# Optimization experiments

Measured on AMD Instinct MI355X. Metric: run time of the kernel, lower is better.

Reference implementation:

```python
import jax, jax.numpy as jnp
import numpy as np

NUM_HEADS = 32
NUM_GROUP_HEADS = 8
DIM_MODEL = 2048
DIM_K = 64
DIM_V = 64


def setup_inputs() -> dict:
    key = jax.random.key(0)
    ks = jax.random.split(key, 11)
    B, S = 1, 2048
    scale = 0.02
    inp = {
        "queries": jax.random.normal(ks[0], (B, S, DIM_MODEL), jnp.float32),
        "keys": jax.random.normal(ks[1], (B, S, DIM_MODEL), jnp.float32),
        "values": jax.random.normal(ks[2], (B, S, DIM_MODEL), jnp.float32),
        "Wq": jax.random.normal(ks[3], (DIM_MODEL, DIM_K * NUM_HEADS), jnp.float32) * scale,
        "bq": jnp.zeros((DIM_K * NUM_HEADS,), jnp.float32),
        "Wk": jax.random.normal(ks[4], (DIM_MODEL, DIM_K * NUM_GROUP_HEADS), jnp.float32) * scale,
        "bk": jnp.zeros((DIM_K * NUM_GROUP_HEADS,), jnp.float32),
        "Wv": jax.random.normal(ks[5], (DIM_MODEL, DIM_V * NUM_GROUP_HEADS), jnp.float32) * scale,
        "bv": jnp.zeros((DIM_V * NUM_GROUP_HEADS,), jnp.float32),
        "Wo": jax.random.normal(ks[6], (DIM_V * NUM_HEADS, DIM_MODEL), jnp.float32) * scale,
        "bo": jnp.zeros((DIM_MODEL,), jnp.float32),
    }
    return inp


def reference(queries, keys, values, Wq, bq, Wk, bk, Wv, bv, Wo, bo):
    B, Sq, _ = queries.shape
    _, Sk, _ = keys.shape
    H, G = NUM_HEADS, NUM_GROUP_HEADS
    repeats = H // G

    # projections -> [B, heads, S, d]
    q = (queries @ Wq + bq).reshape(B, Sq, H, DIM_K).transpose(0, 2, 1, 3)
    k = (keys @ Wk + bk).reshape(B, Sk, G, DIM_K).transpose(0, 2, 1, 3)
    v = (values @ Wv + bv).reshape(B, Sk, G, DIM_V).transpose(0, 2, 1, 3)

    # GQA: repeat each group head `repeats` times (repeat_interleave on head dim)
    k = jnp.repeat(k, repeats, axis=1)  # [B, H, Sk, dk]
    v = jnp.repeat(v, repeats, axis=1)  # [B, H, Sk, dv]

    scores = jnp.einsum("bhqd,bhkd->bhqk", q, k) / (DIM_K ** 0.5)
    causal = jnp.triu(jnp.ones((Sq, Sk), dtype=bool), k=1)
    scores = jnp.where(causal, -jnp.inf, scores)
    attn = jax.nn.softmax(scores, axis=-1)
    out = jnp.einsum("bhqk,bhkd->bhqd", attn, v)  # [B, H, Sq, dv]
    out = out.transpose(0, 2, 1, 3).reshape(B, Sq, H * DIM_V)
    return out @ Wo + bo
```

## Files before the change

### kernel.cpp

```cpp
#include <hip/hip_runtime.h>
#include <hip/hip_bf16.h>

#define S_LEN  2048
#define DMODEL 2048
#define NH     32
#define NG     8
#define DK     64
#define DV     64

typedef short bf16x8 __attribute__((ext_vector_type(8)));
typedef float f32x4  __attribute__((ext_vector_type(4)));

__device__ __forceinline__ ushort f32_to_bf16(float f) {
    uint u = __float_as_uint(f);
    return (ushort)((u + 0x7fffu + ((u >> 16) & 1u)) >> 16);
}
__device__ __forceinline__ float bf16_to_f32(ushort h) {
    return __uint_as_float(((uint)h) << 16);
}

__global__ void cast_f32_to_bf16(const float* __restrict__ in,
                                 ushort* __restrict__ out, int n8) {
    int i = blockIdx.x * blockDim.x + threadIdx.x;
    const int stride = gridDim.x * blockDim.x;
    for (; i < n8; i += stride) {
        const float4 a = ((const float4*)in)[2 * i];
        const float4 b = ((const float4*)in)[2 * i + 1];
        uint4 o;
        o.x = (uint)f32_to_bf16(a.x) | ((uint)f32_to_bf16(a.y) << 16);
        o.y = (uint)f32_to_bf16(a.z) | ((uint)f32_to_bf16(a.w) << 16);
        o.z = (uint)f32_to_bf16(b.x) | ((uint)f32_to_bf16(b.y) << 16);
        o.w = (uint)f32_to_bf16(b.z) | ((uint)f32_to_bf16(b.w) << 16);
        ((uint4*)out)[i] = o;
    }
}

__global__ void transpose_cast_bf16(const float* __restrict__ W,
                                    ushort* __restrict__ Wt, int K, int N) {
    __shared__ float t[32][33];
    const int n0 = blockIdx.x * 32, k0 = blockIdx.y * 32;
    const int tx = threadIdx.x, ty = threadIdx.y;
#pragma unroll
    for (int i = 0; i < 4; ++i)
        t[ty + 8 * i][tx] = W[(size_t)(k0 + ty + 8 * i) * N + n0 + tx];
    __syncthreads();
#pragma unroll
    for (int i = 0; i < 4; ++i)
        Wt[(size_t)(n0 + ty + 8 * i) * K + k0 + tx] = f32_to_bf16(t[tx][ty + 8 * i]);
}

__global__ void transpose_bf16(const ushort* __restrict__ in,
                               ushort* __restrict__ out, int R, int C) {
    __shared__ ushort t[32][34];
    const int c0 = blockIdx.x * 32, r0 = blockIdx.y * 32;
    const int tx = threadIdx.x, ty = threadIdx.y;
#pragma unroll
    for (int i = 0; i < 4; ++i)
        t[ty + 8 * i][tx] = in[(size_t)(r0 + ty + 8 * i) * C + c0 + tx];
    __syncthreads();
#pragma unroll
    for (int i = 0; i < 4; ++i)
        out[(size_t)(c0 + ty + 8 * i) * R + r0 + tx] = t[tx][ty + 8 * i];
}

template <bool OUT_F32>
__device__ __forceinline__ void gemm_body_128x64(
        const ushort* __restrict__ A, const ushort* __restrict__ Bt,
        const float* __restrict__ bias, void* __restrict__ Cv,
        ushort* As, ushort* Bs, int N, int K) {
    const int tid  = threadIdx.x;
    const int lane = tid & 63, wave = tid >> 6;
    const int l15 = lane & 15, quad = lane >> 4;
    const int row0 = blockIdx.y * 128, col0 = blockIdx.x * 64;

    f32x4 acc[2][4];
#pragma unroll
    for (int i = 0; i < 2; ++i)
#pragma unroll
        for (int j = 0; j < 4; ++j) { f32x4 z = {0.f,0.f,0.f,0.f}; acc[i][j] = z; }

    const int ar = tid >> 1, ak = (tid & 1) * 16;
    const int br = tid >> 2, bk = (tid & 3) * 8;
    const ushort* aptr = A  + (size_t)(row0 + ar) * K + ak;
    const ushort* bptr = Bt + (size_t)(col0 + br) * K + bk;

    bf16x8 a0 = *(const bf16x8*)(aptr);
    bf16x8 a1 = *(const bf16x8*)(aptr + 8);
    bf16x8 b0 = *(const bf16x8*)(bptr);

    for (int k0 = 0; k0 < K; k0 += 32) {
        __syncthreads();
        *(bf16x8*)&As[ar * 40 + ak]     = a0;
        *(bf16x8*)&As[ar * 40 + ak + 8] = a1;
        *(bf16x8*)&Bs[br * 40 + bk]     = b0;
        __syncthreads();

        if (k0 + 32 < K) {
            a0 = *(const bf16x8*)(aptr + k0 + 32);
            a1 = *(const bf16x8*)(aptr + k0 + 40);
            b0 = *(const bf16x8*)(bptr + k0 + 32);
        }

        bf16x8 af[2], bf[4];
#pragma unroll
        for (int mi = 0; mi < 2; ++mi)
            af[mi] = *(const bf16x8*)&As[(wave * 32 + mi * 16 + l15) * 40 + quad * 8];
#pragma unroll
        for (int ni = 0; ni < 4; ++ni)
            bf[ni] = *(const bf16x8*)&Bs[(ni * 16 + l15) * 40 + quad * 8];
#pragma unroll
        for (int mi = 0; mi < 2; ++mi)
#pragma unroll
            for (int ni = 0; ni < 4; ++ni)
                acc[mi][ni] = __builtin_amdgcn_mfma_f32_16x16x32_bf16(
                    af[mi], bf[ni], acc[mi][ni], 0, 0, 0);
    }

#pragma unroll
    for (int mi = 0; mi < 2; ++mi)
#pragma unroll
        for (int ni = 0; ni < 4; ++ni) {
            const int col = col0 + ni * 16 + l15;
            const float bv = bias[col];
#pragma unroll
            for (int reg = 0; reg < 4; ++reg) {
                const int row = row0 + wave * 32 + mi * 16 + quad * 4 + reg;
                const float val = acc[mi][ni][reg] + bv;
                if (OUT_F32)
                    ((float*)Cv)[(size_t)row * N + col] = val;
                else
                    ((ushort*)Cv)[(size_t)row * N + col] = f32_to_bf16(val);
            }
        }
}

template <bool OUT_F32>
__global__ __launch_bounds__(256) void gemm_bf16_v2(
        const ushort* __restrict__ A, const ushort* __restrict__ Bt,
        const float* __restrict__ bias, void* __restrict__ Cv, int N, int K) {
    __shared__ ushort As[128 * 40];
    __shared__ ushort Bs[64 * 40];
    gemm_body_128x64<OUT_F32>(A, Bt, bias, Cv, As, Bs, N, K);
}

__global__ __launch_bounds__(256) void gemm_kv(
        const ushort* __restrict__ Xk, const ushort* __restrict__ Xv,
        const ushort* __restrict__ Wkt, const ushort* __restrict__ Wvt,
        const float* __restrict__ bk, const float* __restrict__ bv,
        ushort* __restrict__ Kb, ushort* __restrict__ Vb, int N, int K) {
    __shared__ ushort As[128 * 40];
    __shared__ ushort Bs[64 * 40];
    if (blockIdx.z == 0)
        gemm_body_128x64<false>(Xk, Wkt, bk, Kb, As, Bs, N, K);
    else
        gemm_body_128x64<false>(Xv, Wvt, bv, Vb, As, Bs, N, K);
}

__global__ __launch_bounds__(256) void gqa_attn_mfma(
        const ushort* __restrict__ Qb, const ushort* __restrict__ Kb,
        const ushort* __restrict__ Vt, ushort* __restrict__ Ab) {
    __shared__ ushort Ks[64 * 72];
    __shared__ ushort Vs[64 * 72];
    __shared__ ushort Ps[4][16 * 72];

    const int h    = blockIdx.y, g = h >> 2;
    const int tid  = threadIdx.x;
    const int lane = tid & 63, wave = tid >> 6;
    const int l15  = lane & 15, quad = lane >> 4;
    const int NT   = S_LEN / 64;

    const int srow = tid >> 2, sch = tid & 3;
    const ushort* kbase = Kb + (size_t)srow * (NG * DK) + g * DK + sch * 16;
    const ushort* vbase = Vt + (size_t)(g * 64 + srow) * S_LEN + sch * 16;

    for (int sel = 0; sel < 2; ++sel) {
        const int qt = sel ? (NT - 1 - (int)blockIdx.x) : (int)blockIdx.x;
        const int qr = qt * 64 + wave * 16;

        bf16x8 qa0, qa1;
        {
            const size_t base = (size_t)(qr + l15) * (NH * DK) + (size_t)h * DK + quad * 8;
            qa0 = *(const bf16x8*)&Qb[base];
            qa1 = *(const bf16x8*)&Qb[base + 32];
        }

        f32x4 o[4];
#pragma unroll
        for (int dt = 0; dt < 4; ++dt) { f32x4 z = {0.f,0.f,0.f,0.f}; o[dt] = z; }
        float mrow[4] = {-1e30f, -1e30f, -1e30f, -1e30f};
        float lrow[4] = {0.f, 0.f, 0.f, 0.f};

        bf16x8 kr0 = *(const bf16x8*)(kbase);
        bf16x8 kr1 = *(const bf16x8*)(kbase + 8);
        bf16x8 vr0 = *(const bf16x8*)(vbase);
        bf16x8 vr1 = *(const bf16x8*)(vbase + 8);

        for (int jt = 0; jt <= qt; ++jt) {
            __syncthreads();
            *(bf16x8*)&Ks[srow * 72 + sch * 16]     = kr0;
            *(bf16x8*)&Ks[srow * 72 + sch * 16 + 8] = kr1;
            *(bf16x8*)&Vs[srow * 72 + sch * 16]     = vr0;
            *(bf16x8*)&Vs[srow * 72 + sch * 16 + 8] = vr1;
            __syncthreads();

            if (jt < qt) {
                const size_t ko = (size_t)(jt + 1) * 64 * (NG * DK);
                const size_t vo = (size_t)(jt + 1) * 64;
                kr0 = *(const bf16x8*)(kbase + ko);
                kr1 = *(const bf16x8*)(kbase + ko + 8);
                vr0 = *(const bf16x8*)(vbase + vo);
                vr1 = *(const bf16x8*)(vbase + vo + 8);
            }

            f32x4 s[4];
#pragma unroll
            for (int kt = 0; kt < 4; ++kt) {
                const bf16x8 kb0 = *(const bf16x8*)&Ks[(kt * 16 + l15) * 72 + quad * 8];
                const bf16x8 kb1 = *(const bf16x8*)&Ks[(kt * 16 + l15) * 72 + 32 + quad * 8];
                f32x4 acc = {0.f, 0.f, 0.f, 0.f};
                acc = __builtin_amdgcn_mfma_f32_16x16x32_bf16(qa0, kb0, acc, 0, 0, 0);
                acc = __builtin_amdgcn_mfma_f32_16x16x32_bf16(qa1, kb1, acc, 0, 0, 0);
                s[kt] = acc;
            }

            if (jt == qt) {
#pragma unroll
                for (int kt = 0; kt < 4; ++kt)
#pragma unroll
                    for (int r = 0; r < 4; ++r) {
                        const int key = kt * 16 + l15;
                        const int row = wave * 16 + quad * 4 + r;
                        s[kt][r] = (key <= row) ? s[kt][r] * 0.125f : -1e30f;
                    }
            } else {
#pragma unroll
                for (int kt = 0; kt < 4; ++kt)
#pragma unroll
                    for (int r = 0; r < 4; ++r) s[kt][r] *= 0.125f;
            }

            float rmax[4];
#pragma unroll
            for (int r = 0; r < 4; ++r)
                rmax[r] = fmaxf(fmaxf(s[0][r], s[1][r]), fmaxf(s[2][r], s[3][r]));
#pragma unroll
            for (int off = 1; off <= 8; off <<= 1)
#pragma unroll
                for (int r = 0; r < 4; ++r)
                    rmax[r] = fmaxf(rmax[r], __shfl_xor(rmax[r], off, 64));

            float alpha[4];
#pragma unroll
            for (int r = 0; r < 4; ++r) {
                const float mn = fmaxf(mrow[r], rmax[r]);
                alpha[r] = __expf(mrow[r] - mn);
                mrow[r] = mn;
            }

            float p[4][4], rsum[4];
#pragma unroll
            for (int kt = 0; kt < 4; ++kt)
#pragma unroll
                for (int r = 0; r < 4; ++r)
                    p[kt][r] = __expf(s[kt][r] - mrow[r]);
#pragma unroll
            for (int r = 0; r < 4; ++r)
                rsum[r] = (p[0][r] + p[1][r]) + (p[2][r] + p[3][r]);
#pragma unroll
            for (int off = 1; off <= 8; off <<= 1)
#pragma unroll
                for (int r = 0; r < 4; ++r)
                    rsum[r] += __shfl_xor(rsum[r], off, 64);
#pragma unroll
            for (int r = 0; r < 4; ++r)
                lrow[r] = lrow[r] * alpha[r] + rsum[r];
#pragma unroll
            for (int dt = 0; dt < 4; ++dt)
#pragma unroll
                for (int r = 0; r < 4; ++r)
                    o[dt][r] *= alpha[r];

            ushort* Pw = &Ps[wave][0];
#pragma unroll
            for (int kt = 0; kt < 4; ++kt)
#pragma unroll
                for (int r = 0; r < 4; ++r)
                    Pw[(quad * 4 + r) * 72 + kt * 16 + l15] = f32_to_bf16(p[kt][r]);
            const bf16x8 pa0 = *(const bf16x8*)&Pw[l15 * 72 + quad * 8];
            const bf16x8 pa1 = *(const bf16x8*)&Pw[l15 * 72 + 32 + quad * 8];

#pragma unroll
            for (int dt = 0; dt < 4; ++dt) {
                const bf16x8 vb0 = *(const bf16x8*)&Vs[(dt * 16 + l15) * 72 + quad * 8];
                const bf16x8 vb1 = *(const bf16x8*)&Vs[(dt * 16 + l15) * 72 + 32 + quad * 8];
                o[dt] = __builtin_amdgcn_mfma_f32_16x16x32_bf16(pa0, vb0, o[dt], 0, 0, 0);
                o[dt] = __builtin_amdgcn_mfma_f32_16x16x32_bf16(pa1, vb1, o[dt], 0, 0, 0);
            }
        }

        float inv[4];
#pragma unroll
        for (int r = 0; r < 4; ++r) inv[r] = 1.0f / lrow[r];
#pragma unroll
        for (int dt = 0; dt < 4; ++dt)
#pragma unroll
            for (int r = 0; r < 4; ++r)
                Ab[(size_t)(qr + quad * 4 + r) * (NH * DV) + (size_t)h * DV + dt * 16 + l15] =
                    f32_to_bf16(o[dt][r] * inv[r]);
    }
}

extern "C" void kernel_launch(void* const* d_in, const int* in_sizes, int n_in,
                              void* d_out, int out_size, void* d_ws, size_t ws_size,
                              hipStream_t stream) {
    const float* queries = (const float*)d_in[0];
    const float* keys    = (const float*)d_in[1];
    const float* values  = (const float*)d_in[2];
    const float* Wq      = (const float*)d_in[3];
    const float* bq      = (const float*)d_in[4];
    const float* Wk      = (const float*)d_in[5];
    const float* bk      = (const float*)d_in[6];
    const float* Wv      = (const float*)d_in[7];
    const float* bv      = (const float*)d_in[8];
    const float* Wo      = (const float*)d_in[9];
    const float* bo      = (const float*)d_in[10];
    float* out = (float*)d_out;

    const size_t MB = 1024 * 1024;
    unsigned char* w = (unsigned char*)d_ws;
    ushort* Xq  = (ushort*)(w + 0 * MB);
    ushort* Xk  = (ushort*)(w + 8 * MB);
    ushort* Xv  = (ushort*)(w + 16 * MB);
    ushort* Wqt = (ushort*)(w + 24 * MB);
    ushort* Wkt = (ushort*)(w + 32 * MB);
    ushort* Wvt = (ushort*)(w + 34 * MB);
    ushort* Wot = (ushort*)(w + 36 * MB);
    ushort* Qb  = (ushort*)(w + 44 * MB);
    ushort* Kb  = (ushort*)(w + 52 * MB);
    ushort* Vb  = (ushort*)(w + 54 * MB);
    ushort* Ab  = (ushort*)(w + 56 * MB);
    ushort* Vtp = (ushort*)(w + 8 * MB);

    const int n8 = (S_LEN * DMODEL) / 8;
    cast_f32_to_bf16<<<1024, 256, 0, stream>>>(queries, Xq, n8);
    cast_f32_to_bf16<<<1024, 256, 0, stream>>>(keys,    Xk, n8);
    cast_f32_to_bf16<<<1024, 256, 0, stream>>>(values,  Xv, n8);

    dim3 tb(32, 8);
    transpose_cast_bf16<<<dim3(2048 / 32, 2048 / 32), tb, 0, stream>>>(Wq, Wqt, DMODEL, 2048);
    transpose_cast_bf16<<<dim3(512 / 32,  2048 / 32), tb, 0, stream>>>(Wk, Wkt, DMODEL, 512);
    transpose_cast_bf16<<<dim3(512 / 32,  2048 / 32), tb, 0, stream>>>(Wv, Wvt, DMODEL, 512);
    transpose_cast_bf16<<<dim3(2048 / 32, 2048 / 32), tb, 0, stream>>>(Wo, Wot, DMODEL, 2048);

    gemm_bf16_v2<false><<<dim3(2048 / 64, 2048 / 128), 256, 0, stream>>>(
        Xq, Wqt, bq, Qb, 2048, DMODEL);
    gemm_kv<<<dim3(512 / 64, 2048 / 128, 2), 256, 0, stream>>>(
        Xk, Xv, Wkt, Wvt, bk, bv, Kb, Vb, 512, DMODEL);

    transpose_bf16<<<dim3(512 / 32, 2048 / 32), tb, 0, stream>>>(Vb, Vtp, S_LEN, 512);

    gqa_attn_mfma<<<dim3(16, 32), 256, 0, stream>>>(Qb, Kb, Vtp, Ab);

    gemm_bf16_v2<true><<<dim3(2048 / 64, 2048 / 128), 256, 0, stream>>>(
        Ab, Wot, bo, out, 2048, DMODEL);
}
```

Before: 324.2 us.

## Batch launches, fuse V transpose into GEMM, widen attention key tiles

Merges the three input casts and the four weight transposes into batched launches, and merges the Q/K/V projections into one grid. The V projection now writes its output transposed directly, so the separate transpose kernel goes away. The attention kernel processes 128-key chunks instead of 64 and uses exp2 with a folded log2e scale, which cuts loop iterations and barriers. The cost is larger LDS use and more registers per thread, which could reduce occupancy. The 128-key chunking also does wasted masked work on the diagonal tile.

```diff
diff --git a/kernel.cpp b/kernel.cpp
--- a/kernel.cpp
+++ b/kernel.cpp
@@ -15,12 +15,15 @@
     uint u = __float_as_uint(f);
     return (ushort)((u + 0x7fffu + ((u >> 16) & 1u)) >> 16);
 }
-__device__ __forceinline__ float bf16_to_f32(ushort h) {
-    return __uint_as_float(((uint)h) << 16);
-}
-
-__global__ void cast_f32_to_bf16(const float* __restrict__ in,
-                                 ushort* __restrict__ out, int n8) {
+
+__global__ void cast3_f32_to_bf16(const float* __restrict__ q,
+                                  const float* __restrict__ k,
+                                  const float* __restrict__ v,
+                                  ushort* __restrict__ oq,
+                                  ushort* __restrict__ ok,
+                                  ushort* __restrict__ ov, int n8) {
+    const float* in = blockIdx.z == 0 ? q : (blockIdx.z == 1 ? k : v);
+    ushort* out     = blockIdx.z == 0 ? oq : (blockIdx.z == 1 ? ok : ov);
     int i = blockIdx.x * blockDim.x + threadIdx.x;
     const int stride = gridDim.x * blockDim.x;
     for (; i < n8; i += stride) {
@@ -35,9 +38,12 @@
     }
 }
 
-__global__ void transpose_cast_bf16(const float* __restrict__ W,
-                                    ushort* __restrict__ Wt, int K, int N) {
+__global__ void transpose_cast2(const float* __restrict__ W0, ushort* __restrict__ T0,
+                                const float* __restrict__ W1, ushort* __restrict__ T1,
+                                int K, int N) {
     __shared__ float t[32][33];
+    const float* W = blockIdx.z ? W1 : W0;
+    ushort*     Wt = blockIdx.z ? T1 : T0;
     const int n0 = blockIdx.x * 32, k0 = blockIdx.y * 32;
     const int tx = threadIdx.x, ty = threadIdx.y;
 #pragma unroll
@@ -49,21 +55,7 @@
         Wt[(size_t)(n0 + ty + 8 * i) * K + k0 + tx] = f32_to_bf16(t[tx][ty + 8 * i]);
 }
 
-__global__ void transpose_bf16(const ushort* __restrict__ in,
-                               ushort* __restrict__ out, int R, int C) {
-    __shared__ ushort t[32][34];
-    const int c0 = blockIdx.x * 32, r0 = blockIdx.y * 32;
-    const int tx = threadIdx.x, ty = threadIdx.y;
-#pragma unroll
-    for (int i = 0; i < 4; ++i)
-        t[ty + 8 * i][tx] = in[(size_t)(r0 + ty + 8 * i) * C + c0 + tx];
-    __syncthreads();
-#pragma unroll
-    for (int i = 0; i < 4; ++i)
-        out[(size_t)(c0 + ty + 8 * i) * R + r0 + tx] = t[tx][ty + 8 * i];
-}
-
-template <bool OUT_F32>
+template <int MODE>
 __device__ __forceinline__ void gemm_body_128x64(
         const ushort* __restrict__ A, const ushort* __restrict__ Bt,
         const float* __restrict__ bias, void* __restrict__ Cv,
@@ -122,46 +114,63 @@
         for (int ni = 0; ni < 4; ++ni) {
             const int col = col0 + ni * 16 + l15;
             const float bv = bias[col];
-#pragma unroll
-            for (int reg = 0; reg < 4; ++reg) {
-                const int row = row0 + wave * 32 + mi * 16 + quad * 4 + reg;
-                const float val = acc[mi][ni][reg] + bv;
-                if (OUT_F32)
-                    ((float*)Cv)[(size_t)row * N + col] = val;
-                else
-                    ((ushort*)Cv)[(size_t)row * N + col] = f32_to_bf16(val);
-            }
-        }
-}
-
-template <bool OUT_F32>
-__global__ __launch_bounds__(256) void gemm_bf16_v2(
-        const ushort* __restrict__ A, const ushort* __restrict__ Bt,
-        const float* __restrict__ bias, void* __restrict__ Cv, int N, int K) {
+            float val[4];
+#pragma unroll
+            for (int reg = 0; reg < 4; ++reg)
+                val[reg] = acc[mi][ni][reg] + bv;
+            const int row = row0 + wave * 32 + mi * 16 + quad * 4;
+            if (MODE == 0) {
+#pragma unroll
+                for (int reg = 0; reg < 4; ++reg)
+                    ((ushort*)Cv)[(size_t)(row + reg) * N + col] = f32_to_bf16(val[reg]);
+            } else if (MODE == 1) {
+#pragma unroll
+                for (int reg = 0; reg < 4; ++reg)
+                    ((float*)Cv)[(size_t)(row + reg) * N + col] = val[reg];
+            } else {
+                uint2 u;
+                u.x = (uint)f32_to_bf16(val[0]) | ((uint)f32_to_bf16(val[1]) << 16);
+                u.y = (uint)f32_to_bf16(val[2]) | ((uint)f32_to_bf16(val[3]) << 16);
+                *(uint2*)&((ushort*)Cv)[(size_t)col * S_LEN + row] = u;
+            }
+        }
+}
+
+__global__ __launch_bounds__(256) void gemm_qkv(
+        const ushort* __restrict__ Xq, const ushort* __restrict__ Xk,
+        const ushort* __restrict__ Xv, const ushort* __restrict__ Wqt,
+        const ushort* __restrict__ Wkt, const ushort* __restrict__ Wvt,
+        const float* __restrict__ bq, const float* __restrict__ bk,
+        const float* __restrict__ bv, ushort* __restrict__ Qb,
+        ushort* __restrict__ Kb, ushort* __restrict__ Vtp) {
+    const int z = blockIdx.z;
+    if (z != 0 && blockIdx.x >= 8) return;
     __shared__ ushort As[128 * 40];
     __shared__ ushort Bs[64 * 40];
-    gemm_body_128x64<OUT_F32>(A, Bt, bias, Cv, As, Bs, N, K);
-}
-
-__global__ __launch_bounds__(256) void gemm_kv(
-        const ushort* __restrict__ Xk, const ushort* __restrict__ Xv,
-        const ushort* __restrict__ Wkt, const ushort* __restrict__ Wvt,
-        const float* __restrict__ bk, const float* __restrict__ bv,
-        ushort* __restrict__ Kb, ushort* __restrict__ Vb, int N, int K) {
+    if (z == 0)
+        gemm_body_128x64<0>(Xq, Wqt, bq, Qb, As, Bs, 2048, DMODEL);
+    else if (z == 1)
+        gemm_body_128x64<0>(Xk, Wkt, bk, Kb, As, Bs, 512, DMODEL);
+    else
+        gemm_body_128x64<2>(Xv, Wvt, bv, Vtp, As, Bs, 512, DMODEL);
+}
+
+__global__ __launch_bounds__(256) void gemm_out(
+        const ushort* __restrict__ A, const ushort* __restrict__ Bt,
+        const float* __restrict__ bias, float* __restrict__ C, int N, int K) {
     __shared__ ushort As[128 * 40];
     __shared__ ushort Bs[64 * 40];
-    if (blockIdx.z == 0)
-        gemm_body_128x64<false>(Xk, Wkt, bk, Kb, As, Bs, N, K);
-    else
-        gemm_body_128x64<false>(Xv, Wvt, bv, Vb, As, Bs, N, K);
-}
+    gemm_body_128x64<1>(A, Bt, bias, C, As, Bs, N, K);
+}
+
+#define SC_LOG2 (0.125f * 1.4426950408889634f)
 
 __global__ __launch_bounds__(256) void gqa_attn_mfma(
         const ushort* __restrict__ Qb, const ushort* __restrict__ Kb,
         const ushort* __restrict__ Vt, ushort* __restrict__ Ab) {
-    __shared__ ushort Ks[64 * 72];
-    __shared__ ushort Vs[64 * 72];
-    __shared__ ushort Ps[4][16 * 72];
+    __shared__ ushort Ks[128 * 72];
+    __shared__ ushort Vs[64 * 136];
+    __shared__ ushort Ps[4][16 * 136];
 
     const int h    = blockIdx.y, g = h >> 2;
     const int tid  = threadIdx.x;
@@ -169,13 +178,15 @@
     const int l15  = lane & 15, quad = lane >> 4;
     const int NT   = S_LEN / 64;
 
-    const int srow = tid >> 2, sch = tid & 3;
-    const ushort* kbase = Kb + (size_t)srow * (NG * DK) + g * DK + sch * 16;
-    const ushort* vbase = Vt + (size_t)(g * 64 + srow) * S_LEN + sch * 16;
+    const int krow = tid >> 1, kd = (tid & 1) * 32;
+    const int vrow = tid >> 2, vk = (tid & 3) * 32;
+    const ushort* kbase = Kb + (size_t)krow * (NG * DK) + g * DK + kd;
+    const ushort* vbase = Vt + (size_t)(g * 64 + vrow) * S_LEN + vk;
 
     for (int sel = 0; sel < 2; ++sel) {
         const int qt = sel ? (NT - 1 - (int)blockIdx.x) : (int)blockIdx.x;
         const int qr = qt * 64 + wave * 16;
+        const int nch = (qt >> 1) + 1;
 
         bf16x8 qa0, qa1;
         {
@@ -190,31 +201,35 @@
         float mrow[4] = {-1e30f, -1e30f, -1e30f, -1e30f};
         float lrow[4] = {0.f, 0.f, 0.f, 0.f};
 
-        bf16x8 kr0 = *(const bf16x8*)(kbase);
-        bf16x8 kr1 = *(const bf16x8*)(kbase + 8);
-        bf16x8 vr0 = *(const bf16x8*)(vbase);
-        bf16x8 vr1 = *(const bf16x8*)(vbase + 8);
-
-        for (int jt = 0; jt <= qt; ++jt) {
+        bf16x8 kr[4], vr[4];
+#pragma unroll
+        for (int i = 0; i < 4; ++i) {
+            kr[i] = *(const bf16x8*)(kbase + i * 8);
+            vr[i] = *(const bf16x8*)(vbase + i * 8);
+        }
+
+        for (int c = 0; c < nch; ++c) {
             __syncthreads();
-            *(bf16x8*)&Ks[srow * 72 + sch * 16]     = kr0;
-            *(bf16x8*)&Ks[srow * 72 + sch * 16 + 8] = kr1;
-            *(bf16x8*)&Vs[srow * 72 + sch * 16]     = vr0;
-            *(bf16x8*)&Vs[srow * 72 + sch * 16 + 8] = vr1;
+#pragma unroll
+            for (int i = 0; i < 4; ++i) {
+                *(bf16x8*)&Ks[krow * 72 + kd + i * 8]  = kr[i];
+                *(bf16x8*)&Vs[vrow * 136 + vk + i * 8] = vr[i];
+            }
             __syncthreads();
 
-            if (jt < qt) {
-                const size_t ko = (size_t)(jt + 1) * 64 * (NG * DK);
-                const size_t vo = (size_t)(jt + 1) * 64;
-                kr0 = *(const bf16x8*)(kbase + ko);
-                kr1 = *(const bf16x8*)(kbase + ko + 8);
-                vr0 = *(const bf16x8*)(vbase + vo);
-                vr1 = *(const bf16x8*)(vbase + vo + 8);
-            }
-
-            f32x4 s[4];
-#pragma unroll
-            for (int kt = 0; kt < 4; ++kt) {
+            if (c + 1 < nch) {
+                const size_t ko = (size_t)(c + 1) * 128 * (NG * DK);
+                const size_t vo = (size_t)(c + 1) * 128;
+#pragma unroll
+                for (int i = 0; i < 4; ++i) {
+                    kr[i] = *(const bf16x8*)(kbase + ko + i * 8);
+                    vr[i] = *(const bf16x8*)(vbase + vo + i * 8);
+                }
+            }
+
+            f32x4 s[8];
+#pragma unroll
+            for (int kt = 0; kt < 8; ++kt) {
                 const bf16x8 kb0 = *(const bf16x8*)&Ks[(kt * 16 + l15) * 72 + quad * 8];
                 const bf16x8 kb1 = *(const bf16x8*)&Ks[(kt * 16 + l15) * 72 + 32 + quad * 8];
                 f32x4 acc = {0.f, 0.f, 0.f, 0.f};
@@ -223,26 +238,29 @@
                 s[kt] = acc;
             }
 
-            if (jt == qt) {
-#pragma unroll
-                for (int kt = 0; kt < 4; ++kt)
+            if (c == nch - 1) {
+#pragma unroll
+                for (int kt = 0; kt < 8; ++kt)
 #pragma unroll
                     for (int r = 0; r < 4; ++r) {
-                        const int key = kt * 16 + l15;
-                        const int row = wave * 16 + quad * 4 + r;
-                        s[kt][r] = (key <= row) ? s[kt][r] * 0.125f : -1e30f;
+                        const int key = c * 128 + kt * 16 + l15;
+                        const int row = qr + quad * 4 + r;
+                        s[kt][r] = (key <= row) ? s[kt][r] * SC_LOG2 : -1e30f;
                     }
             } else {
 #pragma unroll
-                for (int kt = 0; kt < 4; ++kt)
-#pragma unroll
-                    for (int r = 0; r < 4; ++r) s[kt][r] *= 0.125f;
+                for (int kt = 0; kt < 8; ++kt)
+#pragma unroll
+                    for (int r = 0; r < 4; ++r) s[kt][r] *= SC_LOG2;
             }
 
             float rmax[4];
 #pragma unroll
-            for (int r = 0; r < 4; ++r)
-                rmax[r] = fmaxf(fmaxf(s[0][r], s[1][r]), fmaxf(s[2][r], s[3][r]));
+            for (int r = 0; r < 4; ++r) {
+                float m01 = fmaxf(s[0][r], s[1][r]), m23 = fmaxf(s[2][r], s[3][r]);
+                float m45 = fmaxf(s[4][r], s[5][r]), m67 = fmaxf(s[6][r], s[7][r]);
+                rmax[r] = fmaxf(fmaxf(m01, m23), fmaxf(m45, m67));
+            }
 #pragma unroll
             for (int off = 1; off <= 8; off <<= 1)
 #pragma unroll
@@ -253,19 +271,20 @@
 #pragma unroll
             for (int r = 0; r < 4; ++r) {
                 const float mn = fmaxf(mrow[r], rmax[r]);
-                alpha[r] = __expf(mrow[r] - mn);
+                alpha[r] = exp2f(mrow[r] - mn);
                 mrow[r] = mn;
             }
 
-            float p[4][4], rsum[4];
-#pragma unroll
-            for (int kt = 0; kt < 4; ++kt)
-#pragma unroll
-                for (int r = 0; r < 4; ++r)
-                    p[kt][r] = __expf(s[kt][r] - mrow[r]);
+            float rsum[4];
+#pragma unroll
+            for (int kt = 0; kt < 8; ++kt)
+#pragma unroll
+                for (int r = 0; r < 4; ++r)
+                    s[kt][r] = exp2f(s[kt][r] - mrow[r]);
 #pragma unroll
             for (int r = 0; r < 4; ++r)
-                rsum[r] = (p[0][r] + p[1][r]) + (p[2][r] + p[3][r]);
+                rsum[r] = ((s[0][r] + s[1][r]) + (s[2][r] + s[3][r]))
+                        + ((s[4][r] + s[5][r]) + (s[6][r] + s[7][r]));
 #pragma unroll
             for (int off = 1; off <= 8; off <<= 1)
 #pragma unroll
@@ -282,20 +301,23 @@
 
             ushort* Pw = &Ps[wave][0];
 #pragma unroll
-            for (int kt = 0; kt < 4; ++kt)
-#pragma unroll
-                for (int r = 0; r < 4; ++r)
-                    Pw[(quad * 4 + r) * 72 + kt * 16 + l15] = f32_to_bf16(p[kt][r]);
-            const bf16x8 pa0 = *(const bf16x8*)&Pw[l15 * 72 + quad * 8];
-            const bf16x8 pa1 = *(const bf16x8*)&Pw[l15 * 72 + 32 + quad * 8];
-
-#pragma unroll
-            for (int dt = 0; dt < 4; ++dt) {
-                const bf16x8 vb0 = *(const bf16x8*)&Vs[(dt * 16 + l15) * 72 + quad * 8];
-                const bf16x8 vb1 = *(const bf16x8*)&Vs[(dt * 16 + l15) * 72 + 32 + quad * 8];
-                o[dt] = __builtin_amdgcn_mfma_f32_16x16x32_bf16(pa0, vb0, o[dt], 0, 0, 0);
-                o[dt] = __builtin_amdgcn_mfma_f32_16x16x32_bf16(pa1, vb1, o[dt], 0, 0, 0);
-            }
+            for (int kt = 0; kt < 8; ++kt)
+#pragma unroll
+                for (int r = 0; r < 4; ++r)
+                    Pw[(quad * 4 + r) * 136 + kt * 16 + l15] = f32_to_bf16(s[kt][r]);
+            bf16x8 pa[4];
+#pragma unroll
+            for (int ks = 0; ks < 4; ++ks)
+                pa[ks] = *(const bf16x8*)&Pw[l15 * 136 + ks * 32 + quad * 8];
+
+#pragma unroll
+            for (int dt = 0; dt < 4; ++dt)
+#pragma unroll
+                for (int ks = 0; ks < 4; ++ks) {
+                    const bf16x8 vb =
+                        *(const bf16x8*)&Vs[(dt * 16 + l15) * 136 + ks * 32 + quad * 8];
+                    o[dt] = __builtin_amdgcn_mfma_f32_16x16x32_bf16(pa[ks], vb, o[dt], 0, 0, 0);
+                }
         }
 
         float inv[4];
@@ -307,6 +329,7 @@
             for (int r = 0; r < 4; ++r)
                 Ab[(size_t)(qr + quad * 4 + r) * (NH * DV) + (size_t)h * DV + dt * 16 + l15] =
                     f32_to_bf16(o[dt][r] * inv[r]);
+        __syncthreads();
     }
 }
 
@@ -337,30 +360,23 @@
     ushort* Wot = (ushort*)(w + 36 * MB);
     ushort* Qb  = (ushort*)(w + 44 * MB);
     ushort* Kb  = (ushort*)(w + 52 * MB);
-    ushort* Vb  = (ushort*)(w + 54 * MB);
+    ushort* Vtp = (ushort*)(w + 54 * MB);
     ushort* Ab  = (ushort*)(w + 56 * MB);
-    ushort* Vtp = (ushort*)(w + 8 * MB);
 
     const int n8 = (S_LEN * DMODEL) / 8;
-    cast_f32_to_bf16<<<1024, 256, 0, stream>>>(queries, Xq, n8);
-    cast_f32_to_bf16<<<1024, 256, 0, stream>>>(keys,    Xk, n8);
-    cast_f32_to_bf16<<<1024, 256, 0, stream>>>(values,  Xv, n8);
+    cast3_f32_to_bf16<<<dim3(512, 1, 3), 256, 0, stream>>>(
+        queries, keys, values, Xq, Xk, Xv, n8);
 
     dim3 tb(32, 8);
-    transpose_cast_bf16<<<dim3(2048 / 32, 2048 / 32), tb, 0, stream>>>(Wq, Wqt, DMODEL, 2048);
-    transpose_cast_bf16<<<dim3(512 / 32,  2048 / 32), tb, 0, stream>>>(Wk, Wkt, DMODEL, 512);
-    transpose_cast_bf16<<<dim3(512 / 32,  2048 / 32), tb, 0, stream>>>(Wv, Wvt, DMODEL, 512);
-    transpose_cast_bf16<<<dim3(2048 / 32, 2048 / 32), tb, 0, stream>>>(Wo, Wot, DMODEL, 2048);
-
-    gemm_bf16_v2<false><<<dim3(2048 / 64, 2048 / 128), 256, 0, stream>>>(
-        Xq, Wqt, bq, Qb, 2048, DMODEL);
-    gemm_kv<<<dim3(512 / 64, 2048 / 128, 2), 256, 0, stream>>>(
-        Xk, Xv, Wkt, Wvt, bk, bv, Kb, Vb, 512, DMODEL);
-
-    transpose_bf16<<<dim3(512 / 32, 2048 / 32), tb, 0, stream>>>(Vb, Vtp, S_LEN, 512);
+    transpose_cast2<<<dim3(2048 / 32, 2048 / 32, 2), tb, 0, stream>>>(
+        Wq, Wqt, Wo, Wot, DMODEL, 2048);
+    transpose_cast2<<<dim3(512 / 32, 2048 / 32, 2), tb, 0, stream>>>(
+        Wk, Wkt, Wv, Wvt, DMODEL, 512);
+
+    gemm_qkv<<<dim3(32, 16, 3), 256, 0, stream>>>(
+        Xq, Xk, Xv, Wqt, Wkt, Wvt, bq, bk, bv, Qb, Kb, Vtp);
 
     gqa_attn_mfma<<<dim3(16, 32), 256, 0, stream>>>(Qb, Kb, Vtp, Ab);
 
-    gemm_bf16_v2<true><<<dim3(2048 / 64, 2048 / 128), 256, 0, stream>>>(
-        Ab, Wot, bo, out, 2048, DMODEL);
-}
+    gemm_out<<<dim3(32, 16), 256, 0, stream>>>(Ab, Wot, bo, out, 2048, DMODEL);
+}
```

Result: slower. 336.0 us (+3.7%).
